# Kernel tuning notes

Hardware: AMD Instinct MI355X
Metric: run time of the kernel (lower is better)

The kernel has to match this reference:

```python
import jax, jax.numpy as jnp
import numpy as np

NUM_HEADS = 16
THETA = 10000.0


def apply_rope(x, positions, theta=THETA):
    # x: [B, H, S, d_k], positions: [B, S] (broadcast over heads)
    d_k = x.shape[-1]
    inv_freq = theta ** (-jnp.arange(0, d_k // 2, dtype=jnp.float32) * 2.0 / d_k)  # [d_k/2]
    ang = positions[:, None, :, None].astype(jnp.float32) * inv_freq  # [B,1,S,d_k/2]
    cos, sin = jnp.cos(ang), jnp.sin(ang)
    x1 = x[..., 0::2]
    x2 = x[..., 1::2]
    r1 = x1 * cos - x2 * sin
    r2 = x1 * sin + x2 * cos
    # interleave back: [..., d_k/2, 2] -> [..., d_k]
    return jnp.stack([r1, r2], axis=-1).reshape(x.shape)


def setup_inputs() -> dict:
    key = jax.random.key(0)
    ks = jax.random.split(key, 5)
    B, S, D = 1, 4096, 1024
    scale = 1.0 / np.sqrt(D)
    x = jax.random.normal(ks[0], (B, S, D), dtype=jnp.float32)
    Wq = jax.random.normal(ks[1], (D, D), dtype=jnp.float32) * scale
    Wk = jax.random.normal(ks[2], (D, D), dtype=jnp.float32) * scale
    Wv = jax.random.normal(ks[3], (D, D), dtype=jnp.float32) * scale
    Wo = jax.random.normal(ks[4], (D, D), dtype=jnp.float32) * scale
    token_positions = jnp.broadcast_to(jnp.arange(S, dtype=jnp.int32), (B, S))
    return {"x": x, "token_positions": token_positions, "Wq": Wq, "Wk": Wk, "Wv": Wv, "Wo": Wo}


def reference(x, token_positions, Wq, Wk, Wv, Wo):
    B, S, D = x.shape
    H = NUM_HEADS
    d_k = D // H
    # fused QKV projection (Linear: y = x @ W^T, no bias)
    q = jnp.einsum('bsd,ed->bse', x, Wq)
    k = jnp.einsum('bsd,ed->bse', x, Wk)
    v = jnp.einsum('bsd,ed->bse', x, Wv)
    # [B,S,H*dk] -> [B,H,S,dk]
    Q = q.reshape(B, S, H, d_k).transpose(0, 2, 1, 3)
    K = k.reshape(B, S, H, d_k).transpose(0, 2, 1, 3)
    V = v.reshape(B, S, H, d_k).transpose(0, 2, 1, 3)
    Q = apply_rope(Q, token_positions)
    K = apply_rope(K, token_positions)
    scores = jnp.einsum('bhqd,bhkd->bhqk', Q, K) / jnp.sqrt(jnp.float32(d_k))
    causal = jnp.tril(jnp.ones((S, S), dtype=bool))
    scores = jnp.where(causal, scores, -jnp.inf)
    P = jax.nn.softmax(scores, axis=-1)
    out = jnp.einsum('bhqk,bhkd->bhqd', P, V)  # [B,H,S,dk]
    out = out.transpose(0, 2, 1, 3).reshape(B, S, D)
    return jnp.einsum('bsd,ed->bse', out, Wo)
```

## Files before the change

### kernel.cpp

```cpp
#include <hip/hip_runtime.h>
#include <hip/hip_bf16.h>
#include <stdint.h>
#include <math.h>

#define S_LEN   4096
#define D_MODEL 1024
#define NHEAD   16
#define DK      64

typedef __attribute__((ext_vector_type(8)))  __bf16 bf16x8;
typedef __attribute__((ext_vector_type(4)))  float  f32x4;
typedef __attribute__((ext_vector_type(16))) float  f32x16;
typedef __attribute__((ext_vector_type(4)))  unsigned int u32x4;
using bf16 = __hip_bfloat16;

__device__ __forceinline__ void load_lds16(const bf16* g, bf16* l) {
    __builtin_amdgcn_global_load_lds(
        (const __attribute__((address_space(1))) void*)g,
        (__attribute__((address_space(3))) void*)l, 16, 0, 0);
}

__global__ void cvt_all(const float* __restrict__ x,
                        const float* __restrict__ w0, const float* __restrict__ w1,
                        const float* __restrict__ w2, const float* __restrict__ w3,
                        bf16* __restrict__ xb,
                        bf16* __restrict__ b0, bf16* __restrict__ b1,
                        bf16* __restrict__ b2, bf16* __restrict__ b3)
{
    size_t i4 = ((size_t)blockIdx.x * 256 + threadIdx.x) * 4;
    const float* s; bf16* d; size_t off;
    const size_t NX = (size_t)S_LEN * D_MODEL;
    const size_t NW = (size_t)D_MODEL * D_MODEL;
    if (i4 < NX) { s = x; d = xb; off = i4; }
    else {
        size_t j = i4 - NX;
        int sel = (int)(j >> 20);
        off = j & (NW - 1);
        s = sel == 0 ? w0 : sel == 1 ? w1 : sel == 2 ? w2 : w3;
        d = sel == 0 ? b0 : sel == 1 ? b1 : sel == 2 ? b2 : b3;
    }
    float4 v = *(const float4*)&s[off];
    bf16 t[4] __attribute__((aligned(8)));
    t[0] = __float2bfloat16(v.x); t[1] = __float2bfloat16(v.y);
    t[2] = __float2bfloat16(v.z); t[3] = __float2bfloat16(v.w);
    *(uint64_t*)&d[off] = *(const uint64_t*)t;
}

__global__ __launch_bounds__(256) void qkv_gemm(
    const bf16* __restrict__ Xb,
    const bf16* __restrict__ Wq, const bf16* __restrict__ Wk, const bf16* __restrict__ Wv,
    const int* __restrict__ pos,
    bf16* __restrict__ Qb, bf16* __restrict__ Kb, bf16* __restrict__ VtG)
{
    const int K = D_MODEL, N = D_MODEL;
    int z = blockIdx.z;
    const bf16* B = (z == 0) ? Wq : (z == 1) ? Wk : Wv;

    __shared__ __align__(16) bf16 As[2][128 * 32];
    __shared__ __align__(16) bf16 Bs[2][128 * 32];
    __shared__ __align__(16) bf16 Ts[4][64 * 24];

    int row0 = blockIdx.y * 128;
    int col0 = blockIdx.x * 128;
    int tid  = threadIdx.x;
    int wv   = tid >> 6, lane = tid & 63;
    int m16  = lane & 15, quad = lane >> 4;
    int wr   = (wv >> 1) * 64, wc = (wv & 1) * 64;
    int l4   = lane >> 2, l3 = (lane & 3) * 8;

    const bf16* ga_base = Xb + (size_t)(row0 + wv * 16 + l4) * K + l3;
    const bf16* gb_base = B  + (size_t)(col0 + wv * 16 + l4) * K + l3;

    auto stage = [&](int k0, int buf) {
        load_lds16(ga_base + k0,            &As[buf][wv * 512]);
        load_lds16(ga_base + k0 + 64 * K,   &As[buf][2048 + wv * 512]);
        load_lds16(gb_base + k0,            &Bs[buf][wv * 512]);
        load_lds16(gb_base + k0 + 64 * K,   &Bs[buf][2048 + wv * 512]);
    };

    f32x4 acc[4][4];
    #pragma unroll
    for (int i = 0; i < 4; i++)
        #pragma unroll
        for (int j = 0; j < 4; j++) acc[i][j] = (f32x4){0.f, 0.f, 0.f, 0.f};

    stage(0, 0);
    for (int k0 = 0; k0 < K; k0 += 32) {
        __syncthreads();
        int buf = (k0 >> 5) & 1;
        if (k0 + 32 < K) stage(k0 + 32, buf ^ 1);
        bf16x8 a[4], b[4];
        #pragma unroll
        for (int mi = 0; mi < 4; mi++) a[mi] = *(const bf16x8*)&As[buf][(wr + mi * 16 + m16) * 32 + quad * 8];
        #pragma unroll
        for (int ni = 0; ni < 4; ni++) b[ni] = *(const bf16x8*)&Bs[buf][(wc + ni * 16 + m16) * 32 + quad * 8];
        #pragma unroll
        for (int mi = 0; mi < 4; mi++)
            #pragma unroll
            for (int ni = 0; ni < 4; ni++)
                acc[mi][ni] = __builtin_amdgcn_mfma_f32_16x16x32_bf16(a[mi], b[ni], acc[mi][ni], 0, 0, 0);
    }

    if (z < 2) {
        bf16* O = (z == 0) ? Qb : Kb;
        const float qscale = (z == 0) ? 0.18033688011112042f : 1.0f;
        float invf[4];
        #pragma unroll
        for (int ni = 0; ni < 4; ni++) {
            float fi = (float)((ni * 16 + m16) >> 1);
            invf[ni] = exp2f(fi * (-0.41524101186092028f));
        }
        bool odd = (m16 & 1) != 0;
        #pragma unroll
        for (int mi = 0; mi < 4; mi++) {
            #pragma unroll
            for (int r = 0; r < 4; r++) {
                int gr = row0 + wr + mi * 16 + quad * 4 + r;
                float p = (float)pos[gr];
                #pragma unroll
                for (int ni = 0; ni < 4; ni++) {
                    float own   = acc[mi][ni][r];
                    float other = __shfl_xor(own, 1);
                    float sn, cs;
                    __sincosf(p * invf[ni], &sn, &cs);
                    float x1 = odd ? other : own;
                    float x2 = odd ? own   : other;
                    float res = odd ? (x1 * sn + x2 * cs) : (x1 * cs - x2 * sn);
                    int gc = col0 + wc + ni * 16 + m16;
                    O[(size_t)gr * N + gc] = __float2bfloat16(res * qscale);
                }
            }
        }
    } else {
        #pragma unroll
        for (int mi = 0; mi < 4; mi++) {
            #pragma unroll
            for (int nt = 0; nt < 4; nt++) {
                bf16 t4[4] __attribute__((aligned(8)));
                #pragma unroll
                for (int r = 0; r < 4; r++) t4[r] = __float2bfloat16(acc[mi][nt][r]);
                *(uint64_t*)&Ts[wv][(nt * 16 + m16) * 24 + quad * 4] = *(const uint64_t*)t4;
            }
            #pragma unroll
            for (int rep = 0; rep < 2; rep++) {
                int c  = (lane >> 1) + rep * 32;
                int r8 = lane & 1;
                bf16x8 val = *(const bf16x8*)&Ts[wv][c * 24 + r8 * 8];
                int gc = col0 + wc + c;
                int gr = row0 + wr + mi * 16 + r8 * 8;
                *(bf16x8*)&VtG[(size_t)gc * S_LEN + gr] = val;
            }
        }
    }
}

__global__ __launch_bounds__(256) void out_gemm(
    const bf16* __restrict__ A_, const bf16* __restrict__ B,
    float* __restrict__ C)
{
    const int K = D_MODEL, N = D_MODEL;
    __shared__ __align__(16) bf16 As[2][128 * 32];
    __shared__ __align__(16) bf16 Bs[2][64 * 32];

    int row0 = blockIdx.y * 128;
    int col0 = blockIdx.x * 64;
    int tid  = threadIdx.x;
    int wv   = tid >> 6, lane = tid & 63;
    int m16  = lane & 15, quad = lane >> 4;
    int wr   = (wv >> 1) * 64, wc = (wv & 1) * 32;
    int l4   = lane >> 2, l3 = (lane & 3) * 8;

    const bf16* ga_base = A_ + (size_t)(row0 + wv * 16 + l4) * K + l3;
    const bf16* gb_base = B  + (size_t)(col0 + wv * 16 + l4) * K + l3;

    auto stage = [&](int k0, int buf) {
        load_lds16(ga_base + k0,            &As[buf][wv * 512]);
        load_lds16(ga_base + k0 + 64 * K,   &As[buf][2048 + wv * 512]);
        load_lds16(gb_base + k0,            &Bs[buf][wv * 512]);
    };

    f32x4 acc[4][2];
    #pragma unroll
    for (int i = 0; i < 4; i++)
        #pragma unroll
        for (int j = 0; j < 2; j++) acc[i][j] = (f32x4){0.f, 0.f, 0.f, 0.f};

    stage(0, 0);
    for (int k0 = 0; k0 < K; k0 += 32) {
        __syncthreads();
        int buf = (k0 >> 5) & 1;
        if (k0 + 32 < K) stage(k0 + 32, buf ^ 1);
        bf16x8 a[4], b[2];
        #pragma unroll
        for (int mi = 0; mi < 4; mi++) a[mi] = *(const bf16x8*)&As[buf][(wr + mi * 16 + m16) * 32 + quad * 8];
        #pragma unroll
        for (int ni = 0; ni < 2; ni++) b[ni] = *(const bf16x8*)&Bs[buf][(wc + ni * 16 + m16) * 32 + quad * 8];
        #pragma unroll
        for (int mi = 0; mi < 4; mi++)
            #pragma unroll
            for (int ni = 0; ni < 2; ni++)
                acc[mi][ni] = __builtin_amdgcn_mfma_f32_16x16x32_bf16(a[mi], b[ni], acc[mi][ni], 0, 0, 0);
    }

    #pragma unroll
    for (int mi = 0; mi < 4; mi++)
        #pragma unroll
        for (int ni = 0; ni < 2; ni++)
            #pragma unroll
            for (int r = 0; r < 4; r++) {
                int gr = row0 + wr + mi * 16 + quad * 4 + r;
                int gc = col0 + wc + ni * 16 + m16;
                C[(size_t)gr * N + gc] = acc[mi][ni][r];
            }
}

__global__ __launch_bounds__(256, 4) void attn_kernel(
    const bf16* __restrict__ Qb, const bf16* __restrict__ Kb, const bf16* __restrict__ VtG,
    bf16* __restrict__ Attn)
{
    int bx  = blockIdx.x;
    int h   = bx & 15;
    int qt  = 63 - (bx >> 4);
    int tid = threadIdx.x;
    int wv  = tid >> 6, lane = tid & 63;
    int wq  = wv >> 1, wp = wv & 1;
    int l31 = lane & 31, hi = lane >> 5;
    int hc  = h * DK;
    int qs  = qt * 64 + wq * 32;
    int myq = qs + l31;

    int krow = (l31 & 19) | (((l31 >> 3) & 1) << 2) | (((l31 >> 2) & 1) << 3);
    int k7   = krow & 7;
    int d7   = l31 & 7;

    __shared__ __align__(16) bf16 KT[2][4096];
    __shared__ __align__(16) bf16 VT[2][4096];
    __shared__ float Lbuf[2][2][32];

    int srow = lane >> 3, schunk = (lane & 7) ^ srow;
    const bf16* kst = Kb  + (size_t)(wv * 16 + srow) * D_MODEL + hc + schunk * 8;
    const bf16* vst = VtG + (size_t)(hc + wv * 16 + srow) * S_LEN + schunk * 8;

    auto stage = [&](int t, int buf) {
        size_t kb64 = (size_t)t * 64;
        #pragma unroll
        for (int i = 0; i < 2; i++) {
            load_lds16(kst + (kb64 + 8 * i) * D_MODEL, &KT[buf][(wv * 16 + 8 * i) * 64]);
            load_lds16(vst + (size_t)(8 * i) * S_LEN + kb64, &VT[buf][(wv * 16 + 8 * i) * 64]);
        }
    };

    const bf16* qbase = Qb + (size_t)(qs + l31) * D_MODEL + hc + hi * 8;
    bf16x8 aQ[4];
    #pragma unroll
    for (int d = 0; d < 4; d++) aQ[d] = *(const bf16x8*)&qbase[d * 16];

    f32x16 o0, o1;
    #pragma unroll
    for (int i = 0; i < 16; i++) { o0[i] = 0.f; o1[i] = 0.f; }
    float l_part = 0.f;

    auto tile = [&](int buf, int kb, bool diag) {
        const bf16* ktb = &KT[buf][(wp * 32 + krow) * 64];
        bf16x8 aK[4];
        #pragma unroll
        for (int ks = 0; ks < 4; ks++)
            aK[ks] = *(const bf16x8*)&ktb[(((ks * 2 + hi) ^ k7)) * 8];

        f32x16 s;
        #pragma unroll
        for (int i = 0; i < 16; i++) s[i] = 0.f;
        s = __builtin_amdgcn_mfma_f32_32x32x16_bf16(aK[0], aQ[0], s, 0, 0, 0);
        s = __builtin_amdgcn_mfma_f32_32x32x16_bf16(aK[1], aQ[1], s, 0, 0, 0);
        s = __builtin_amdgcn_mfma_f32_32x32x16_bf16(aK[2], aQ[2], s, 0, 0, 0);
        s = __builtin_amdgcn_mfma_f32_32x32x16_bf16(aK[3], aQ[3], s, 0, 0, 0);

        float p[16];
        #pragma unroll
        for (int r = 0; r < 16; r++) {
            float pv = __builtin_amdgcn_exp2f(s[r] - 8.0f);
            if (diag) {
                int key = kb + (r & 3) + ((r >> 2) & 1) * 4 + hi * 8 + (r >> 3) * 16;
                if (key > myq) pv = 0.f;
            }
            l_part += pv;
            p[r] = pv;
        }

        unsigned int w[8];
        #pragma unroll
        for (int i = 0; i < 8; i++)
            asm("v_cvt_pk_bf16_f32 %0, %1, %2" : "=v"(w[i]) : "v"(p[2 * i]), "v"(p[2 * i + 1]));
        u32x4 wa = {w[0], w[1], w[2], w[3]};
        u32x4 wb = {w[4], w[5], w[6], w[7]};
        bf16x8 aP0 = __builtin_bit_cast(bf16x8, wa);
        bf16x8 aP1 = __builtin_bit_cast(bf16x8, wb);

        bf16x8 bV00 = *(const bf16x8*)&VT[buf][(l31)      * 64 + ((wp * 4 + 0 + hi) ^ d7) * 8];
        bf16x8 bV10 = *(const bf16x8*)&VT[buf][(l31)      * 64 + ((wp * 4 + 2 + hi) ^ d7) * 8];
        bf16x8 bV01 = *(const bf16x8*)&VT[buf][(32 + l31) * 64 + ((wp * 4 + 0 + hi) ^ d7) * 8];
        bf16x8 bV11 = *(const bf16x8*)&VT[buf][(32 + l31) * 64 + ((wp * 4 + 2 + hi) ^ d7) * 8];

        o0 = __builtin_amdgcn_mfma_f32_32x32x16_bf16(aP0, bV00, o0, 0, 0, 0);
        o0 = __builtin_amdgcn_mfma_f32_32x32x16_bf16(aP1, bV10, o0, 0, 0, 0);
        o1 = __builtin_amdgcn_mfma_f32_32x32x16_bf16(aP0, bV01, o1, 0, 0, 0);
        o1 = __builtin_amdgcn_mfma_f32_32x32x16_bf16(aP1, bV11, o1, 0, 0, 0);
    };

    stage(0, 0);
    for (int t = 0; t <= qt; ++t) {
        __syncthreads();
        int buf = t & 1;
        if (t < qt) stage(t + 1, buf ^ 1);
        int kb = t * 64 + wp * 32;
        if (kb <= qs) tile(buf, kb, kb == qs);
    }

    __syncthreads();
    float lt = l_part + __shfl_xor(l_part, 32);
    float* Obuf = (float*)&KT[0][0];
    if (wp == 1) {
        #pragma unroll
        for (int r = 0; r < 16; r++) {
            Obuf[((wq * 2 + 0) * 16 + r) * 64 + lane] = o0[r];
            Obuf[((wq * 2 + 1) * 16 + r) * 64 + lane] = o1[r];
        }
    }
    if (lane < 32) Lbuf[wq][wp][l31] = lt;
    __syncthreads();
    if (wp == 0) {
        #pragma unroll
        for (int r = 0; r < 16; r++) {
            int qr = (r & 3) + (r >> 2) * 8 + hi * 4;
            float lsum = Lbuf[wq][0][qr] + Lbuf[wq][1][qr];
            float inv  = 1.0f / lsum;
            float v0 = (o0[r] + Obuf[((wq * 2 + 0) * 16 + r) * 64 + lane]) * inv;
            float v1 = (o1[r] + Obuf[((wq * 2 + 1) * 16 + r) * 64 + lane]) * inv;
            bf16* dst = Attn + (size_t)(qs + qr) * D_MODEL + hc + l31;
            dst[0]  = __float2bfloat16(v0);
            dst[32] = __float2bfloat16(v1);
        }
    }
}

extern "C" void kernel_launch(void* const* d_in, const int* in_sizes, int n_in,
                              void* d_out, int out_size, void* d_ws, size_t ws_size,
                              hipStream_t stream)
{
    const float* x  = (const float*)d_in[0];
    const int*   pos= (const int*)d_in[1];
    const float* Wq = (const float*)d_in[2];
    const float* Wk = (const float*)d_in[3];
    const float* Wv = (const float*)d_in[4];
    const float* Wo = (const float*)d_in[5];
    float* out = (float*)d_out;

    char* ws = (char*)d_ws;
    bf16*  xb   = (bf16*) (ws);
    bf16*  wqb  = (bf16*) (ws + ( 8ull << 20));
    bf16*  wkb  = (bf16*) (ws + (10ull << 20));
    bf16*  wvb  = (bf16*) (ws + (12ull << 20));
    bf16*  wob  = (bf16*) (ws + (14ull << 20));
    bf16*  Qb   = (bf16*) (ws + (16ull << 20));
    bf16*  Kb   = (bf16*) (ws + (24ull << 20));
    bf16*  VtG  = (bf16*) (ws + (32ull << 20));
    bf16*  Attn = (bf16*) (ws + (40ull << 20));

    cvt_all<<<8192, 256, 0, stream>>>(x, Wq, Wk, Wv, Wo, xb, wqb, wkb, wvb, wob);

    qkv_gemm<<<dim3(8, 32, 3), 256, 0, stream>>>(xb, wqb, wkb, wvb, pos, Qb, Kb, VtG);

    attn_kernel<<<dim3(1024), 256, 0, stream>>>(Qb, Kb, VtG, Attn);

    out_gemm<<<dim3(16, 32), 256, 0, stream>>>(Attn, wob, out);
}
```

Measured before the change: 212.5 us.

## Compute softmax row sums via MFMA with ones vector and unroll double-buffer loop

Replaces the per-lane scalar accumulation of softmax denominators with two extra MFMAs that multiply P by a vector of ones, so the row sums come out directly from the matrix unit in bf16-rounded form. The K/V loop is manually unrolled by two so buffer pointers and swizzled LDS offsets are hoisted as constants. The -8 bias is folded into the score accumulator's initial value, and the RoPE frequency exp2 uses the hardware intrinsic. This adds two MFMAs per tile and changes the sum to use bf16-rounded probabilities, trading scalar VALU adds and the cross-lane shuffle for matrix work.

```diff
diff --git a/kernel.cpp b/kernel.cpp
--- a/kernel.cpp
+++ b/kernel.cpp
@@ -108,7 +108,7 @@
         #pragma unroll
         for (int ni = 0; ni < 4; ni++) {
             float fi = (float)((ni * 16 + m16) >> 1);
-            invf[ni] = exp2f(fi * (-0.41524101186092028f));
+            invf[ni] = __builtin_amdgcn_exp2f(fi * (-0.41524101186092028f));
         }
         bool odd = (m16 & 1) != 0;
         #pragma unroll
@@ -250,26 +250,38 @@
         }
     };
 
+    const bf16* ktb0 = &KT[0][(wp * 32 + krow) * 64];
+    const bf16* ktb1 = &KT[1][(wp * 32 + krow) * 64];
+    const bf16* vtb0 = &VT[0][l31 * 64];
+    const bf16* vtb1 = &VT[1][l31 * 64];
+    int koff[4];
+    #pragma unroll
+    for (int ks = 0; ks < 4; ks++) koff[ks] = ((ks * 2 + hi) ^ k7) * 8;
+    int voff0 = ((wp * 4 + 0 + hi) ^ d7) * 8;
+    int voff2 = ((wp * 4 + 2 + hi) ^ d7) * 8;
+
     const bf16* qbase = Qb + (size_t)(qs + l31) * D_MODEL + hc + hi * 8;
     bf16x8 aQ[4];
     #pragma unroll
     for (int d = 0; d < 4; d++) aQ[d] = *(const bf16x8*)&qbase[d * 16];
 
-    f32x16 o0, o1;
-    #pragma unroll
-    for (int i = 0; i < 16; i++) { o0[i] = 0.f; o1[i] = 0.f; }
-    float l_part = 0.f;
-
-    auto tile = [&](int buf, int kb, bool diag) {
-        const bf16* ktb = &KT[buf][(wp * 32 + krow) * 64];
+    bf16x8 bone;
+    #pragma unroll
+    for (int j = 0; j < 8; j++) bone[j] = (__bf16)1.0f;
+
+    f32x16 o0, o1, o_sum;
+    #pragma unroll
+    for (int i = 0; i < 16; i++) { o0[i] = 0.f; o1[i] = 0.f; o_sum[i] = 0.f; }
+
+    auto tile = [&](const bf16* ktb, const bf16* vtb, int kb, bool diag) {
         bf16x8 aK[4];
         #pragma unroll
         for (int ks = 0; ks < 4; ks++)
-            aK[ks] = *(const bf16x8*)&ktb[(((ks * 2 + hi) ^ k7)) * 8];
+            aK[ks] = *(const bf16x8*)&ktb[koff[ks]];
 
         f32x16 s;
         #pragma unroll
-        for (int i = 0; i < 16; i++) s[i] = 0.f;
+        for (int i = 0; i < 16; i++) s[i] = -8.0f;
         s = __builtin_amdgcn_mfma_f32_32x32x16_bf16(aK[0], aQ[0], s, 0, 0, 0);
         s = __builtin_amdgcn_mfma_f32_32x32x16_bf16(aK[1], aQ[1], s, 0, 0, 0);
         s = __builtin_amdgcn_mfma_f32_32x32x16_bf16(aK[2], aQ[2], s, 0, 0, 0);
@@ -278,12 +290,11 @@
         float p[16];
         #pragma unroll
         for (int r = 0; r < 16; r++) {
-            float pv = __builtin_amdgcn_exp2f(s[r] - 8.0f);
+            float pv = __builtin_amdgcn_exp2f(s[r]);
             if (diag) {
                 int key = kb + (r & 3) + ((r >> 2) & 1) * 4 + hi * 8 + (r >> 3) * 16;
                 if (key > myq) pv = 0.f;
             }
-            l_part += pv;
             p[r] = pv;
         }
 
@@ -296,28 +307,42 @@
         bf16x8 aP0 = __builtin_bit_cast(bf16x8, wa);
         bf16x8 aP1 = __builtin_bit_cast(bf16x8, wb);
 
-        bf16x8 bV00 = *(const bf16x8*)&VT[buf][(l31)      * 64 + ((wp * 4 + 0 + hi) ^ d7) * 8];
-        bf16x8 bV10 = *(const bf16x8*)&VT[buf][(l31)      * 64 + ((wp * 4 + 2 + hi) ^ d7) * 8];
-        bf16x8 bV01 = *(const bf16x8*)&VT[buf][(32 + l31) * 64 + ((wp * 4 + 0 + hi) ^ d7) * 8];
-        bf16x8 bV11 = *(const bf16x8*)&VT[buf][(32 + l31) * 64 + ((wp * 4 + 2 + hi) ^ d7) * 8];
+        bf16x8 bV00 = *(const bf16x8*)&vtb[voff0];
+        bf16x8 bV10 = *(const bf16x8*)&vtb[voff2];
+        bf16x8 bV01 = *(const bf16x8*)&vtb[voff0 + 32 * 64];
+        bf16x8 bV11 = *(const bf16x8*)&vtb[voff2 + 32 * 64];
 
         o0 = __builtin_amdgcn_mfma_f32_32x32x16_bf16(aP0, bV00, o0, 0, 0, 0);
         o0 = __builtin_amdgcn_mfma_f32_32x32x16_bf16(aP1, bV10, o0, 0, 0, 0);
         o1 = __builtin_amdgcn_mfma_f32_32x32x16_bf16(aP0, bV01, o1, 0, 0, 0);
         o1 = __builtin_amdgcn_mfma_f32_32x32x16_bf16(aP1, bV11, o1, 0, 0, 0);
+        o_sum = __builtin_amdgcn_mfma_f32_32x32x16_bf16(aP0, bone, o_sum, 0, 0, 0);
+        o_sum = __builtin_amdgcn_mfma_f32_32x32x16_bf16(aP1, bone, o_sum, 0, 0, 0);
     };
 
     stage(0, 0);
-    for (int t = 0; t <= qt; ++t) {
+    for (int t = 0; t <= qt; t += 2) {
         __syncthreads();
-        int buf = t & 1;
-        if (t < qt) stage(t + 1, buf ^ 1);
-        int kb = t * 64 + wp * 32;
-        if (kb <= qs) tile(buf, kb, kb == qs);
+        if (t < qt) stage(t + 1, 1);
+        {
+            int kb = t * 64 + wp * 32;
+            if (kb <= qs) tile(ktb0, vtb0, kb, kb == qs);
+        }
+        if (t + 1 > qt) break;
+        __syncthreads();
+        if (t + 1 < qt) stage(t + 2, 0);
+        {
+            int kb = (t + 1) * 64 + wp * 32;
+            if (kb <= qs) tile(ktb1, vtb1, kb, kb == qs);
+        }
     }
 
     __syncthreads();
-    float lt = l_part + __shfl_xor(l_part, 32);
+    #pragma unroll
+    for (int r = 0; r < 16; r++) {
+        int qr = (r & 3) + (r >> 2) * 8 + hi * 4;
+        Lbuf[wq][wp][qr] = o_sum[r];
+    }
     float* Obuf = (float*)&KT[0][0];
     if (wp == 1) {
         #pragma unroll
@@ -326,7 +351,6 @@
             Obuf[((wq * 2 + 1) * 16 + r) * 64 + lane] = o1[r];
         }
     }
-    if (lane < 32) Lbuf[wq][wp][l31] = lt;
     __syncthreads();
     if (wp == 0) {
         #pragma unroll
```

Result: faster. 205.6 us (-3.3%).
